# Optimization experiments

Hardware: AMD Instinct MI355X
Metric: run time of the kernel (lower is better)

## Reference

```python
import jax, jax.numpy as jnp
import numpy as np

B, S, H = 2, 512, 768
NH, HD = 12, 64  # num heads, head size


def setup_inputs() -> dict:
    key = jax.random.key(0)
    ks = jax.random.split(key, 11)
    std = 0.02
    return {
        "from_path_hidden": jax.random.normal(ks[0], (B, S, H), jnp.float32),
        "to_path_hidden": jax.random.normal(ks[1], (B, S, H), jnp.float32),
        "attention_mask": jnp.zeros((B, 1, 1, S), jnp.float32),
        "Wq": jax.random.normal(ks[2], (H, H), jnp.float32) * std,
        "bq": jnp.zeros((H,), jnp.float32),
        "Wk": jax.random.normal(ks[3], (H, H), jnp.float32) * std,
        "bk": jnp.zeros((H,), jnp.float32),
        "Wvf": jax.random.normal(ks[4], (H, H), jnp.float32) * std,
        "bvf": jnp.zeros((H,), jnp.float32),
        "Wvt": jax.random.normal(ks[5], (H, H), jnp.float32) * std,
        "bvt": jnp.zeros((H,), jnp.float32),
    }


def _heads(x):
    # [B,S,H] -> [B,NH,S,HD]
    b, s, _ = x.shape
    return x.reshape(b, s, NH, HD).transpose(0, 2, 1, 3)


def reference(from_path_hidden, to_path_hidden, attention_mask,
              Wq, bq, Wk, bk, Wvf, bvf, Wvt, bvt):
    # torch Linear: y = x @ W^T + b
    q = _heads(from_path_hidden @ Wq.T + bq)   # [B,NH,S,HD]
    k = _heads(to_path_hidden @ Wk.T + bk)     # [B,NH,S,HD]
    vf = _heads(from_path_hidden @ Wvf.T + bvf)  # value_from, indexed by query pos
    vt = _heads(to_path_hidden @ Wvt.T + bvt)    # value_to, indexed by key pos

    scores = jnp.einsum("bhqd,bhkd->bhqk", q, k) / jnp.sqrt(jnp.asarray(HD, q.dtype))
    scores = scores + attention_mask  # additive mask, broadcasts [B,1,1,S]
    probs = jax.nn.softmax(scores, axis=-1)  # dropout is identity in eval mode

    # use_expanded_value=True: ctx[b,h,q,:] = sum_k probs[b,h,q,k] * (vf[b,h,q,:] + vt[b,h,k,:])
    # = probs @ vt + (sum_k probs) * vf  -- exact, avoids the [B,NH,S,S,HD] tensor
    ctx = jnp.einsum("bhqk,bhkd->bhqd", probs, vt) + probs.sum(-1, keepdims=True) * vf

    # [B,NH,S,HD] -> [B,S,H]
    ctx = ctx.transpose(0, 2, 1, 3).reshape(from_path_hidden.shape[0], -1, NH * HD)
    return ctx
```

## Files before the change

kernel.cpp:

```cpp
#include <hip/hip_runtime.h>
#include <hip/hip_bf16.h>
#include <math.h>

#define Bq  2
#define Sq  512
#define Hq  768
#define NHq 12
#define HDq 64
#define SHsz (Bq * Sq * Hq)
#define WSZ  (Hq * Hq)

typedef __bf16 bf16x8 __attribute__((ext_vector_type(8)));
typedef unsigned short u16x8 __attribute__((ext_vector_type(8)));
typedef float f32x4 __attribute__((ext_vector_type(4)));

static __device__ __forceinline__ unsigned short f2bf(float f) {
    unsigned int u = __float_as_uint(f);
    u += 0x7fffu + ((u >> 16) & 1u);
    return (unsigned short)(u >> 16);
}
static __device__ __forceinline__ float bf2f(unsigned short v) {
    return __uint_as_float(((unsigned int)v) << 16);
}

static __device__ __forceinline__ f32x4 mfma_bf16(bf16x8 a, bf16x8 b, f32x4 c) {
    return __builtin_amdgcn_mfma_f32_16x16x32_bf16(a, b, c, 0, 0, 0);
}

static __device__ __forceinline__ void async16(const void* g, void* l) {
    __builtin_amdgcn_global_load_lds(
        (const __attribute__((address_space(1))) void*)(uintptr_t)g,
        (__attribute__((address_space(3))) void*)(unsigned int)(uintptr_t)l,
        16, 0, 0);
}

__global__ __launch_bounds__(256) void cvt_kernel(
    const float* __restrict__ from_h, const float* __restrict__ to_h,
    const float* __restrict__ Wq, const float* __restrict__ Wk,
    const float* __restrict__ Wvf, const float* __restrict__ Wvt,
    unsigned short* __restrict__ ws)
{
    const int z = blockIdx.y;
    const float* src; unsigned short* dst; int n;
    switch (z) {
        case 0:  src = from_h; dst = ws + 3 * SHsz;           n = SHsz; break;
        case 1:  src = to_h;   dst = ws + 4 * SHsz;           n = SHsz; break;
        case 2:  src = Wq;     dst = ws + 5 * SHsz;           n = WSZ;  break;
        case 3:  src = Wk;     dst = ws + 5 * SHsz + WSZ;     n = WSZ;  break;
        case 4:  src = Wvf;    dst = ws + 5 * SHsz + 2 * WSZ; n = WSZ;  break;
        default: src = Wvt;    dst = ws + 5 * SHsz + 3 * WSZ; n = WSZ;  break;
    }
    const int idx = (blockIdx.x * 256 + threadIdx.x) * 8;
    if (idx < n) {
        const float4 a = *(const float4*)(src + idx);
        const float4 b = *(const float4*)(src + idx + 4);
        u16x8 o = { f2bf(a.x), f2bf(a.y), f2bf(a.z), f2bf(a.w),
                    f2bf(b.x), f2bf(b.y), f2bf(b.z), f2bf(b.w) };
        *(u16x8*)(dst + idx) = o;
    }
}

__global__ __launch_bounds__(256) void proj_gemm(
    const unsigned short* __restrict__ fbf, const unsigned short* __restrict__ tbf,
    const unsigned short* __restrict__ wqb, const unsigned short* __restrict__ wkb,
    const unsigned short* __restrict__ wvfb, const unsigned short* __restrict__ wvtb,
    const float* __restrict__ bq, const float* __restrict__ bk,
    const float* __restrict__ bvf, const float* __restrict__ bvt,
    unsigned short* __restrict__ qbf, unsigned short* __restrict__ kbf,
    unsigned short* __restrict__ vtt, unsigned short* __restrict__ vfb)
{
    __shared__ unsigned short lds[16384];
    unsigned short* Als = lds;
    unsigned short* Wls = lds + 8192;

    const int z = blockIdx.z;
    const unsigned short *A, *W;
    const float* bias;
    if (z == 0)      { A = fbf; W = wqb;  bias = bq;  }
    else if (z == 1) { A = tbf; W = wkb;  bias = bk;  }
    else if (z == 2) { A = tbf; W = wvtb; bias = bvt; }
    else             { A = fbf; W = wvfb; bias = bvf; }

    const int t    = threadIdx.x;
    const int wv   = t >> 6;
    const int lane = t & 63;
    const int l16  = lane & 15;
    const int quad = lane >> 4;
    const int bn = blockIdx.x;
    const int bm = blockIdx.y;

    const int srow = lane >> 3;
    const int sgrp = (lane & 7) ^ (srow & 7);

    f32x4 acc[4] = {};

    for (int kt = 0; kt < Hq / 128; ++kt) {
        __syncthreads();
        #pragma unroll
        for (int kh = 0; kh < 2; ++kh) {
            const int kc = kt * 128 + kh * 64;
            #pragma unroll
            for (int c = 0; c < 2; ++c) {
                const int r0 = wv * 16 + c * 8;
                async16(A + (size_t)(bm * 64 + r0 + srow) * Hq + kc + sgrp * 8, &Als[kh * 4096 + r0 * 64]);
                async16(W + (size_t)(bn * 64 + r0 + srow) * Hq + kc + sgrp * 8, &Wls[kh * 4096 + r0 * 64]);
            }
        }
        __syncthreads();

        #pragma unroll
        for (int kh = 0; kh < 2; ++kh) {
            #pragma unroll
            for (int kk = 0; kk < 2; ++kk) {
                const int sg = kh * 4096 + ((kk * 4 + quad) ^ (l16 & 7)) * 8;
                const bf16x8 af = *(const bf16x8*)&Als[(wv * 16 + l16) * 64 + sg];
                #pragma unroll
                for (int j = 0; j < 4; ++j) {
                    const bf16x8 bfr = *(const bf16x8*)&Wls[(j * 16 + l16) * 64 + sg];
                    acc[j] = mfma_bf16(af, bfr, acc[j]);
                }
            }
        }
    }

    __syncthreads();

    unsigned short* rep = lds;
    if (z == 2) {
        #pragma unroll
        for (int j = 0; j < 4; ++j) {
            const float bv = bias[bn * 64 + j * 16 + l16];
            #pragma unroll
            for (int r = 0; r < 4; ++r)
                rep[(j * 16 + l16) * 72 + wv * 16 + quad * 4 + r] = f2bf(acc[j][r] + bv);
        }
    } else {
        #pragma unroll
        for (int j = 0; j < 4; ++j) {
            const float bv = bias[bn * 64 + j * 16 + l16];
            #pragma unroll
            for (int r = 0; r < 4; ++r)
                rep[(wv * 16 + quad * 4 + r) * 72 + j * 16 + l16] = f2bf(acc[j][r] + bv);
        }
    }
    __syncthreads();

    const int row = t >> 2;
    #pragma unroll
    for (int p = 0; p < 2; ++p) {
        const int col0 = ((t & 3) + p * 4) * 8;
        const u16x8 v = *(const u16x8*)&rep[row * 72 + col0];
        if (z == 2) {
            const int bb = bm >> 3, m0 = (bm & 7) * 64;
            *(u16x8*)&vtt[((size_t)((bb * NHq + bn) * HDq + row)) * Sq + m0 + col0] = v;
        } else {
            unsigned short* dstp = (z == 0) ? qbf : (z == 1) ? kbf : vfb;
            *(u16x8*)&dstp[(size_t)(bm * 64 + row) * Hq + bn * 64 + col0] = v;
        }
    }
}

__global__ __launch_bounds__(256) void attn_kernel(
    const unsigned short* __restrict__ qbf,
    const unsigned short* __restrict__ kbf,
    const unsigned short* __restrict__ vtt,
    const unsigned short* __restrict__ vfb,
    const float* __restrict__ amask,
    float* __restrict__ outp)
{
    __shared__ unsigned short Plds[4 * 16 * 40];
    __shared__ float Ols[3 * 16 * 68];
    __shared__ float Tls[3 * 16];

    const int t    = threadIdx.x;
    const int wv   = t >> 6;
    const int lane = t & 63;
    const int l16  = lane & 15;
    const int quad = lane >> 4;
    const int q0 = blockIdx.x * 16;
    const int h  = blockIdx.y;
    const int b  = blockIdx.z;

    const unsigned short* qrow = qbf + ((size_t)(b * Sq + q0 + l16)) * Hq + h * HDq + quad * 8;
    const bf16x8 aq0 = *(const bf16x8*)qrow;
    const bf16x8 aq1 = *(const bf16x8*)(qrow + 32);

    f32x4 O[4] = {};
    float ts[4] = {0.f, 0.f, 0.f, 0.f};
    const float scale = 0.125f;
    unsigned short* myP = &Plds[wv * 16 * 40];

    for (int kt = 0; kt < 4; ++kt) {
        const int k0 = wv * 128 + kt * 32;
        const unsigned short* kr = kbf + ((size_t)(b * Sq + k0 + l16)) * Hq + h * HDq + quad * 8;
        const bf16x8 kb00 = *(const bf16x8*)kr;
        const bf16x8 kb01 = *(const bf16x8*)(kr + 32);
        const bf16x8 kb10 = *(const bf16x8*)(kr + 16 * Hq);
        const bf16x8 kb11 = *(const bf16x8*)(kr + 16 * Hq + 32);

        f32x4 s0 = {}, s1 = {};
        s0 = mfma_bf16(aq0, kb00, s0);
        s0 = mfma_bf16(aq1, kb01, s0);
        s1 = mfma_bf16(aq0, kb10, s1);
        s1 = mfma_bf16(aq1, kb11, s1);

        const float mk0 = amask[b * Sq + k0 + l16];
        const float mk1 = amask[b * Sq + k0 + 16 + l16];

        float p0[4], p1[4];
        #pragma unroll
        for (int r = 0; r < 4; ++r) {
            p0[r] = __expf(s0[r] * scale + mk0);
            p1[r] = __expf(s1[r] * scale + mk1);
            ts[r] += p0[r] + p1[r];
        }

        #pragma unroll
        for (int r = 0; r < 4; ++r) {
            myP[(quad * 4 + r) * 40 + l16]      = f2bf(p0[r]);
            myP[(quad * 4 + r) * 40 + 16 + l16] = f2bf(p1[r]);
        }
        const bf16x8 pa = *(const bf16x8*)&myP[l16 * 40 + quad * 8];

        const unsigned short* vr = vtt + ((size_t)((b * NHq + h) * HDq + l16)) * Sq + k0 + quad * 8;
        #pragma unroll
        for (int j = 0; j < 4; ++j) {
            const bf16x8 vb = *(const bf16x8*)(vr + (size_t)j * 16 * Sq);
            O[j] = mfma_bf16(pa, vb, O[j]);
        }
    }

    #pragma unroll
    for (int off = 1; off < 16; off <<= 1)
        #pragma unroll
        for (int r = 0; r < 4; ++r) ts[r] += __shfl_xor(ts[r], off);

    if (wv > 0) {
        float* myO = &Ols[(wv - 1) * 16 * 68];
        #pragma unroll
        for (int j = 0; j < 4; ++j)
            #pragma unroll
            for (int r = 0; r < 4; ++r)
                myO[(quad * 4 + r) * 68 + j * 16 + l16] = O[j][r];
        if (l16 == 0)
            #pragma unroll
            for (int r = 0; r < 4; ++r) Tls[(wv - 1) * 16 + quad * 4 + r] = ts[r];
    }
    __syncthreads();
    if (wv > 0) return;

    #pragma unroll
    for (int r = 0; r < 4; ++r) {
        const int rr = quad * 4 + r;
        const float tot = ts[r] + Tls[rr] + Tls[16 + rr] + Tls[32 + rr];
        const float inv = 1.f / tot;
        const int row = q0 + rr;
        #pragma unroll
        for (int j = 0; j < 4; ++j) {
            const int col = h * HDq + j * 16 + l16;
            const size_t idx = ((size_t)(b * Sq + row)) * Hq + col;
            const float oj = O[j][r]
                + Ols[rr * 68 + j * 16 + l16]
                + Ols[16 * 68 + rr * 68 + j * 16 + l16]
                + Ols[2 * 16 * 68 + rr * 68 + j * 16 + l16];
            outp[idx] = oj * inv + bf2f(vfb[idx]);
        }
    }
}

extern "C" void kernel_launch(void* const* d_in, const int* in_sizes, int n_in,
                              void* d_out, int out_size, void* d_ws, size_t ws_size,
                              hipStream_t stream) {
    (void)in_sizes; (void)n_in; (void)out_size; (void)ws_size;
    const float* from_h = (const float*)d_in[0];
    const float* to_h   = (const float*)d_in[1];
    const float* amask  = (const float*)d_in[2];
    const float* Wq  = (const float*)d_in[3];
    const float* bqv = (const float*)d_in[4];
    const float* Wk  = (const float*)d_in[5];
    const float* bkv = (const float*)d_in[6];
    const float* Wvf = (const float*)d_in[7];
    const float* bvf = (const float*)d_in[8];
    const float* Wvt = (const float*)d_in[9];
    const float* bvt = (const float*)d_in[10];
    float* outp = (float*)d_out;

    unsigned short* ws = (unsigned short*)d_ws;
    unsigned short* qbf = ws;
    unsigned short* kbf = ws + SHsz;
    unsigned short* vtt = ws + 2 * SHsz;
    unsigned short* fbf = ws + 3 * SHsz;
    unsigned short* tbf = ws + 4 * SHsz;
    unsigned short* wqb  = ws + 5 * SHsz;
    unsigned short* wkb  = wqb + WSZ;
    unsigned short* wvfb = wqb + 2 * WSZ;
    unsigned short* wvtb = wqb + 3 * WSZ;
    unsigned short* vfb  = wqb + 4 * WSZ;

    cvt_kernel<<<dim3(384, 6), 256, 0, stream>>>(from_h, to_h, Wq, Wk, Wvf, Wvt, ws);

    dim3 gp(12, 16, 4);
    proj_gemm<<<gp, 256, 0, stream>>>(fbf, tbf, wqb, wkb, wvfb, wvtb,
                                      bqv, bkv, bvf, bvt, qbf, kbf, vtt, vfb);

    dim3 ga(Sq / 16, NHq, Bq);
    attn_kernel<<<ga, 256, 0, stream>>>(qbf, kbf, vtt, vfb, amask, outp);
}
```

Baseline: 107.2 us.

## Fuse convert, projection, and attention into one persistent kernel with grid barriers

Replaces the three separate launches (bf16 conversion, projection GEMM, attention) with a single persistent kernel of 512 blocks. The stages are separated by software grid barriers built on atomic counters and spin-wait, and each stage distributes its work over the blocks in a strided loop. The aim is to remove launch overhead and inter-kernel gaps. In exchange it relies on all 512 blocks being co-resident and adds spin-barrier cost. The barrier has a timeout that could break correctness under contention, and the counter is never reset, relying on rounding to multiples of NBLK.

```diff
diff --git a/kernel.cpp b/kernel.cpp
--- a/kernel.cpp
+++ b/kernel.cpp
@@ -9,6 +9,7 @@
 #define HDq 64
 #define SHsz (Bq * Sq * Hq)
 #define WSZ  (Hq * Hq)
+#define NBLK 512
 
 typedef __bf16 bf16x8 __attribute__((ext_vector_type(8)));
 typedef unsigned short u16x8 __attribute__((ext_vector_type(8)));
@@ -34,236 +35,294 @@
         16, 0, 0);
 }
 
-__global__ __launch_bounds__(256) void cvt_kernel(
+static __device__ __forceinline__ u16x8 cvt8(float4 a, float4 b) {
+    u16x8 o = { f2bf(a.x), f2bf(a.y), f2bf(a.z), f2bf(a.w),
+                f2bf(b.x), f2bf(b.y), f2bf(b.z), f2bf(b.w) };
+    return o;
+}
+
+__device__ unsigned int g_bar[2] = {0u, 0u};
+
+static __device__ __forceinline__ void grid_barrier(int which) {
+    __threadfence();
+    __syncthreads();
+    if (threadIdx.x == 0) {
+        const unsigned int v =
+            __hip_atomic_fetch_add(&g_bar[which], 1u, __ATOMIC_ACQ_REL,
+                                   __HIP_MEMORY_SCOPE_AGENT) + 1u;
+        const unsigned int target = ((v + (NBLK - 1u)) / NBLK) * NBLK;
+        const long long t0 = (long long)__builtin_amdgcn_s_memrealtime();
+        while (__hip_atomic_load(&g_bar[which], __ATOMIC_ACQUIRE,
+                                 __HIP_MEMORY_SCOPE_AGENT) < target) {
+            __builtin_amdgcn_s_sleep(2);
+            if ((long long)__builtin_amdgcn_s_memrealtime() - t0 > 4000000LL) break;
+        }
+    }
+    __syncthreads();
+    __threadfence();
+}
+
+__global__ __launch_bounds__(256, 2) void fused_kernel(
     const float* __restrict__ from_h, const float* __restrict__ to_h,
-    const float* __restrict__ Wq, const float* __restrict__ Wk,
-    const float* __restrict__ Wvf, const float* __restrict__ Wvt,
-    unsigned short* __restrict__ ws)
-{
-    const int z = blockIdx.y;
-    const float* src; unsigned short* dst; int n;
-    switch (z) {
-        case 0:  src = from_h; dst = ws + 3 * SHsz;           n = SHsz; break;
-        case 1:  src = to_h;   dst = ws + 4 * SHsz;           n = SHsz; break;
-        case 2:  src = Wq;     dst = ws + 5 * SHsz;           n = WSZ;  break;
-        case 3:  src = Wk;     dst = ws + 5 * SHsz + WSZ;     n = WSZ;  break;
-        case 4:  src = Wvf;    dst = ws + 5 * SHsz + 2 * WSZ; n = WSZ;  break;
-        default: src = Wvt;    dst = ws + 5 * SHsz + 3 * WSZ; n = WSZ;  break;
-    }
-    const int idx = (blockIdx.x * 256 + threadIdx.x) * 8;
-    if (idx < n) {
-        const float4 a = *(const float4*)(src + idx);
-        const float4 b = *(const float4*)(src + idx + 4);
-        u16x8 o = { f2bf(a.x), f2bf(a.y), f2bf(a.z), f2bf(a.w),
-                    f2bf(b.x), f2bf(b.y), f2bf(b.z), f2bf(b.w) };
-        *(u16x8*)(dst + idx) = o;
-    }
-}
-
-__global__ __launch_bounds__(256) void proj_gemm(
-    const unsigned short* __restrict__ fbf, const unsigned short* __restrict__ tbf,
-    const unsigned short* __restrict__ wqb, const unsigned short* __restrict__ wkb,
-    const unsigned short* __restrict__ wvfb, const unsigned short* __restrict__ wvtb,
-    const float* __restrict__ bq, const float* __restrict__ bk,
-    const float* __restrict__ bvf, const float* __restrict__ bvt,
-    unsigned short* __restrict__ qbf, unsigned short* __restrict__ kbf,
-    unsigned short* __restrict__ vtt, unsigned short* __restrict__ vfb)
+    const float* __restrict__ amask,
+    const float* __restrict__ Wq,  const float* __restrict__ bq,
+    const float* __restrict__ Wk,  const float* __restrict__ bk,
+    const float* __restrict__ Wvf, const float* __restrict__ bvf,
+    const float* __restrict__ Wvt, const float* __restrict__ bvt,
+    float* __restrict__ outp, unsigned short* __restrict__ ws)
 {
     __shared__ unsigned short lds[16384];
-    unsigned short* Als = lds;
-    unsigned short* Wls = lds + 8192;
-
-    const int z = blockIdx.z;
-    const unsigned short *A, *W;
-    const float* bias;
-    if (z == 0)      { A = fbf; W = wqb;  bias = bq;  }
-    else if (z == 1) { A = tbf; W = wkb;  bias = bk;  }
-    else if (z == 2) { A = tbf; W = wvtb; bias = bvt; }
-    else             { A = fbf; W = wvfb; bias = bvf; }
-
-    const int t    = threadIdx.x;
-    const int wv   = t >> 6;
-    const int lane = t & 63;
-    const int l16  = lane & 15;
-    const int quad = lane >> 4;
-    const int bn = blockIdx.x;
-    const int bm = blockIdx.y;
-
-    const int srow = lane >> 3;
-    const int sgrp = (lane & 7) ^ (srow & 7);
-
-    f32x4 acc[4] = {};
-
-    for (int kt = 0; kt < Hq / 128; ++kt) {
+
+    unsigned short* qbf  = ws;
+    unsigned short* kbf  = ws + SHsz;
+    unsigned short* vtt  = ws + 2 * SHsz;
+    unsigned short* fbf  = ws + 3 * SHsz;
+    unsigned short* tbf  = ws + 4 * SHsz;
+    unsigned short* wqb  = ws + 5 * SHsz;
+    unsigned short* vfb  = wqb + 4 * WSZ;
+
+    const int bid = blockIdx.x;
+    const int t   = threadIdx.x;
+
+    if (bid < 128) {
+        const int g0 = bid * 256 + t;
+        #pragma unroll
+        for (int it = 0; it < 3; ++it) {
+            const int idx = (g0 + it * 32768) * 8;
+            const float4 a = *(const float4*)(from_h + idx);
+            const float4 b = *(const float4*)(from_h + idx + 4);
+            *(u16x8*)(fbf + idx) = cvt8(a, b);
+        }
+    } else if (bid < 256) {
+        const int g0 = (bid - 128) * 256 + t;
+        #pragma unroll
+        for (int it = 0; it < 3; ++it) {
+            const int idx = (g0 + it * 32768) * 8;
+            const float4 a = *(const float4*)(to_h + idx);
+            const float4 b = *(const float4*)(to_h + idx + 4);
+            *(u16x8*)(tbf + idx) = cvt8(a, b);
+        }
+    } else {
+        const int g0 = (bid - 256) * 256 + t;
+        #pragma unroll
+        for (int it = 0; it < 4; ++it) {
+            const int c  = g0 + it * 65536;
+            const int wi = c / 73728;
+            const int off = c - wi * 73728;
+            const float* src = (wi == 0) ? Wq : (wi == 1) ? Wk : (wi == 2) ? Wvf : Wvt;
+            const float4 a = *(const float4*)(src + off * 8);
+            const float4 b = *(const float4*)(src + off * 8 + 4);
+            *(u16x8*)(wqb + c * 8) = cvt8(a, b);
+        }
+        if (g0 < 32768) {
+            const int c  = g0 + 262144;
+            const int off = c - 3 * 73728;
+            const float4 a = *(const float4*)(Wvt + off * 8);
+            const float4 b = *(const float4*)(Wvt + off * 8 + 4);
+            *(u16x8*)(wqb + c * 8) = cvt8(a, b);
+        }
+    }
+
+    grid_barrier(0);
+
+    for (int wid = bid; wid < 768; wid += NBLK) {
+        unsigned short* Als = lds;
+        unsigned short* Wls = lds + 8192;
+
+        const int z  = wid / 192;
+        const int r  = wid - z * 192;
+        const int bm = r / 12;
+        const int bn = r - bm * 12;
+
+        const unsigned short *A, *W;
+        const float* bias;
+        if (z == 0)      { A = fbf; W = wqb;           bias = bq;  }
+        else if (z == 1) { A = tbf; W = wqb + WSZ;     bias = bk;  }
+        else if (z == 2) { A = tbf; W = wqb + 3 * WSZ; bias = bvt; }
+        else             { A = fbf; W = wqb + 2 * WSZ; bias = bvf; }
+
+        const int wv   = t >> 6;
+        const int lane = t & 63;
+        const int l16  = lane & 15;
+        const int quad = lane >> 4;
+        const int srow = lane >> 3;
+        const int sgrp = (lane & 7) ^ (srow & 7);
+
+        f32x4 acc[4] = {};
+
+        for (int kt = 0; kt < Hq / 128; ++kt) {
+            __syncthreads();
+            #pragma unroll
+            for (int kh = 0; kh < 2; ++kh) {
+                const int kc = kt * 128 + kh * 64;
+                #pragma unroll
+                for (int c = 0; c < 2; ++c) {
+                    const int r0 = wv * 16 + c * 8;
+                    async16(A + (size_t)(bm * 64 + r0 + srow) * Hq + kc + sgrp * 8, &Als[kh * 4096 + r0 * 64]);
+                    async16(W + (size_t)(bn * 64 + r0 + srow) * Hq + kc + sgrp * 8, &Wls[kh * 4096 + r0 * 64]);
+                }
+            }
+            __syncthreads();
+
+            #pragma unroll
+            for (int kh = 0; kh < 2; ++kh) {
+                #pragma unroll
+                for (int kk = 0; kk < 2; ++kk) {
+                    const int sg = kh * 4096 + ((kk * 4 + quad) ^ (l16 & 7)) * 8;
+                    const bf16x8 af = *(const bf16x8*)&Als[(wv * 16 + l16) * 64 + sg];
+                    #pragma unroll
+                    for (int j = 0; j < 4; ++j) {
+                        const bf16x8 bfr = *(const bf16x8*)&Wls[(j * 16 + l16) * 64 + sg];
+                        acc[j] = mfma_bf16(af, bfr, acc[j]);
+                    }
+                }
+            }
+        }
+
         __syncthreads();
+
+        unsigned short* rep = lds;
+        if (z == 2) {
+            #pragma unroll
+            for (int j = 0; j < 4; ++j) {
+                const float bv = bias[bn * 64 + j * 16 + l16];
+                #pragma unroll
+                for (int r2 = 0; r2 < 4; ++r2)
+                    rep[(j * 16 + l16) * 72 + wv * 16 + quad * 4 + r2] = f2bf(acc[j][r2] + bv);
+            }
+        } else {
+            #pragma unroll
+            for (int j = 0; j < 4; ++j) {
+                const float bv = bias[bn * 64 + j * 16 + l16];
+                #pragma unroll
+                for (int r2 = 0; r2 < 4; ++r2)
+                    rep[(wv * 16 + quad * 4 + r2) * 72 + j * 16 + l16] = f2bf(acc[j][r2] + bv);
+            }
+        }
+        __syncthreads();
+
+        const int row = t >> 2;
         #pragma unroll
-        for (int kh = 0; kh < 2; ++kh) {
-            const int kc = kt * 128 + kh * 64;
-            #pragma unroll
-            for (int c = 0; c < 2; ++c) {
-                const int r0 = wv * 16 + c * 8;
-                async16(A + (size_t)(bm * 64 + r0 + srow) * Hq + kc + sgrp * 8, &Als[kh * 4096 + r0 * 64]);
-                async16(W + (size_t)(bn * 64 + r0 + srow) * Hq + kc + sgrp * 8, &Wls[kh * 4096 + r0 * 64]);
+        for (int p = 0; p < 2; ++p) {
+            const int col0 = ((t & 3) + p * 4) * 8;
+            const u16x8 v = *(const u16x8*)&rep[row * 72 + col0];
+            if (z == 2) {
+                const int bb = bm >> 3, m0 = (bm & 7) * 64;
+                *(u16x8*)&vtt[((size_t)((bb * NHq + bn) * HDq + row)) * Sq + m0 + col0] = v;
+            } else {
+                unsigned short* dstp = (z == 0) ? qbf : (z == 1) ? kbf : vfb;
+                *(u16x8*)&dstp[(size_t)(bm * 64 + row) * Hq + bn * 64 + col0] = v;
             }
         }
         __syncthreads();
-
-        #pragma unroll
-        for (int kh = 0; kh < 2; ++kh) {
-            #pragma unroll
-            for (int kk = 0; kk < 2; ++kk) {
-                const int sg = kh * 4096 + ((kk * 4 + quad) ^ (l16 & 7)) * 8;
-                const bf16x8 af = *(const bf16x8*)&Als[(wv * 16 + l16) * 64 + sg];
+    }
+
+    grid_barrier(1);
+
+    {
+        unsigned short* Plds = lds;
+        float* Ols = (float*)(lds + 2560);
+        float* Tls = (float*)(lds + 2560 + 6528);
+
+        const int wv   = t >> 6;
+        const int lane = t & 63;
+        const int l16  = lane & 15;
+        const int quad = lane >> 4;
+        const float scale = 0.125f;
+        unsigned short* myP = &Plds[wv * 16 * 40];
+
+        for (int wid = bid; wid < 768; wid += NBLK) {
+            __syncthreads();
+
+            const int b  = wid / 384;
+            const int r3 = wid - b * 384;
+            const int h  = r3 >> 5;
+            const int q0 = (r3 & 31) * 16;
+
+            const unsigned short* qrow = qbf + ((size_t)(b * Sq + q0 + l16)) * Hq + h * HDq + quad * 8;
+            const bf16x8 aq0 = *(const bf16x8*)qrow;
+            const bf16x8 aq1 = *(const bf16x8*)(qrow + 32);
+
+            f32x4 O[4] = {};
+            float ts[4] = {0.f, 0.f, 0.f, 0.f};
+
+            for (int kt = 0; kt < 4; ++kt) {
+                const int k0 = wv * 128 + kt * 32;
+                const unsigned short* kr = kbf + ((size_t)(b * Sq + k0 + l16)) * Hq + h * HDq + quad * 8;
+                const bf16x8 kb00 = *(const bf16x8*)kr;
+                const bf16x8 kb01 = *(const bf16x8*)(kr + 32);
+                const bf16x8 kb10 = *(const bf16x8*)(kr + 16 * Hq);
+                const bf16x8 kb11 = *(const bf16x8*)(kr + 16 * Hq + 32);
+
+                f32x4 s0 = {}, s1 = {};
+                s0 = mfma_bf16(aq0, kb00, s0);
+                s0 = mfma_bf16(aq1, kb01, s0);
+                s1 = mfma_bf16(aq0, kb10, s1);
+                s1 = mfma_bf16(aq1, kb11, s1);
+
+                const float mk0 = amask[b * Sq + k0 + l16];
+                const float mk1 = amask[b * Sq + k0 + 16 + l16];
+
+                float p0[4], p1[4];
+                #pragma unroll
+                for (int r2 = 0; r2 < 4; ++r2) {
+                    p0[r2] = __expf(s0[r2] * scale + mk0);
+                    p1[r2] = __expf(s1[r2] * scale + mk1);
+                    ts[r2] += p0[r2] + p1[r2];
+                }
+
+                #pragma unroll
+                for (int r2 = 0; r2 < 4; ++r2) {
+                    myP[(quad * 4 + r2) * 40 + l16]      = f2bf(p0[r2]);
+                    myP[(quad * 4 + r2) * 40 + 16 + l16] = f2bf(p1[r2]);
+                }
+                const bf16x8 pa = *(const bf16x8*)&myP[l16 * 40 + quad * 8];
+
+                const unsigned short* vr = vtt + ((size_t)((b * NHq + h) * HDq + l16)) * Sq + k0 + quad * 8;
                 #pragma unroll
                 for (int j = 0; j < 4; ++j) {
-                    const bf16x8 bfr = *(const bf16x8*)&Wls[(j * 16 + l16) * 64 + sg];
-                    acc[j] = mfma_bf16(af, bfr, acc[j]);
-                }
-            }
-        }
-    }
-
-    __syncthreads();
-
-    unsigned short* rep = lds;
-    if (z == 2) {
-        #pragma unroll
-        for (int j = 0; j < 4; ++j) {
-            const float bv = bias[bn * 64 + j * 16 + l16];
-            #pragma unroll
-            for (int r = 0; r < 4; ++r)
-                rep[(j * 16 + l16) * 72 + wv * 16 + quad * 4 + r] = f2bf(acc[j][r] + bv);
-        }
-    } else {
-        #pragma unroll
-        for (int j = 0; j < 4; ++j) {
-            const float bv = bias[bn * 64 + j * 16 + l16];
-            #pragma unroll
-            for (int r = 0; r < 4; ++r)
-                rep[(wv * 16 + quad * 4 + r) * 72 + j * 16 + l16] = f2bf(acc[j][r] + bv);
-        }
-    }
-    __syncthreads();
-
-    const int row = t >> 2;
-    #pragma unroll
-    for (int p = 0; p < 2; ++p) {
-        const int col0 = ((t & 3) + p * 4) * 8;
-        const u16x8 v = *(const u16x8*)&rep[row * 72 + col0];
-        if (z == 2) {
-            const int bb = bm >> 3, m0 = (bm & 7) * 64;
-            *(u16x8*)&vtt[((size_t)((bb * NHq + bn) * HDq + row)) * Sq + m0 + col0] = v;
-        } else {
-            unsigned short* dstp = (z == 0) ? qbf : (z == 1) ? kbf : vfb;
-            *(u16x8*)&dstp[(size_t)(bm * 64 + row) * Hq + bn * 64 + col0] = v;
-        }
-    }
-}
-
-__global__ __launch_bounds__(256) void attn_kernel(
-    const unsigned short* __restrict__ qbf,
-    const unsigned short* __restrict__ kbf,
-    const unsigned short* __restrict__ vtt,
-    const unsigned short* __restrict__ vfb,
-    const float* __restrict__ amask,
-    float* __restrict__ outp)
-{
-    __shared__ unsigned short Plds[4 * 16 * 40];
-    __shared__ float Ols[3 * 16 * 68];
-    __shared__ float Tls[3 * 16];
-
-    const int t    = threadIdx.x;
-    const int wv   = t >> 6;
-    const int lane = t & 63;
-    const int l16  = lane & 15;
-    const int quad = lane >> 4;
-    const int q0 = blockIdx.x * 16;
-    const int h  = blockIdx.y;
-    const int b  = blockIdx.z;
-
-    const unsigned short* qrow = qbf + ((size_t)(b * Sq + q0 + l16)) * Hq + h * HDq + quad * 8;
-    const bf16x8 aq0 = *(const bf16x8*)qrow;
-    const bf16x8 aq1 = *(const bf16x8*)(qrow + 32);
-
-    f32x4 O[4] = {};
-    float ts[4] = {0.f, 0.f, 0.f, 0.f};
-    const float scale = 0.125f;
-    unsigned short* myP = &Plds[wv * 16 * 40];
-
-    for (int kt = 0; kt < 4; ++kt) {
-        const int k0 = wv * 128 + kt * 32;
-        const unsigned short* kr = kbf + ((size_t)(b * Sq + k0 + l16)) * Hq + h * HDq + quad * 8;
-        const bf16x8 kb00 = *(const bf16x8*)kr;
-        const bf16x8 kb01 = *(const bf16x8*)(kr + 32);
-        const bf16x8 kb10 = *(const bf16x8*)(kr + 16 * Hq);
-        const bf16x8 kb11 = *(const bf16x8*)(kr + 16 * Hq + 32);
-
-        f32x4 s0 = {}, s1 = {};
-        s0 = mfma_bf16(aq0, kb00, s0);
-        s0 = mfma_bf16(aq1, kb01, s0);
-        s1 = mfma_bf16(aq0, kb10, s1);
-        s1 = mfma_bf16(aq1, kb11, s1);
-
-        const float mk0 = amask[b * Sq + k0 + l16];
-        const float mk1 = amask[b * Sq + k0 + 16 + l16];
-
-        float p0[4], p1[4];
-        #pragma unroll
-        for (int r = 0; r < 4; ++r) {
-            p0[r] = __expf(s0[r] * scale + mk0);
-            p1[r] = __expf(s1[r] * scale + mk1);
-            ts[r] += p0[r] + p1[r];
-        }
-
-        #pragma unroll
-        for (int r = 0; r < 4; ++r) {
-            myP[(quad * 4 + r) * 40 + l16]      = f2bf(p0[r]);
-            myP[(quad * 4 + r) * 40 + 16 + l16] = f2bf(p1[r]);
-        }
-        const bf16x8 pa = *(const bf16x8*)&myP[l16 * 40 + quad * 8];
-
-        const unsigned short* vr = vtt + ((size_t)((b * NHq + h) * HDq + l16)) * Sq + k0 + quad * 8;
-        #pragma unroll
-        for (int j = 0; j < 4; ++j) {
-            const bf16x8 vb = *(const bf16x8*)(vr + (size_t)j * 16 * Sq);
-            O[j] = mfma_bf16(pa, vb, O[j]);
-        }
-    }
-
-    #pragma unroll
-    for (int off = 1; off < 16; off <<= 1)
-        #pragma unroll
-        for (int r = 0; r < 4; ++r) ts[r] += __shfl_xor(ts[r], off);
-
-    if (wv > 0) {
-        float* myO = &Ols[(wv - 1) * 16 * 68];
-        #pragma unroll
-        for (int j = 0; j < 4; ++j)
-            #pragma unroll
-            for (int r = 0; r < 4; ++r)
-                myO[(quad * 4 + r) * 68 + j * 16 + l16] = O[j][r];
-        if (l16 == 0)
-            #pragma unroll
-            for (int r = 0; r < 4; ++r) Tls[(wv - 1) * 16 + quad * 4 + r] = ts[r];
-    }
-    __syncthreads();
-    if (wv > 0) return;
-
-    #pragma unroll
-    for (int r = 0; r < 4; ++r) {
-        const int rr = quad * 4 + r;
-        const float tot = ts[r] + Tls[rr] + Tls[16 + rr] + Tls[32 + rr];
-        const float inv = 1.f / tot;
-        const int row = q0 + rr;
-        #pragma unroll
-        for (int j = 0; j < 4; ++j) {
-            const int col = h * HDq + j * 16 + l16;
-            const size_t idx = ((size_t)(b * Sq + row)) * Hq + col;
-            const float oj = O[j][r]
-                + Ols[rr * 68 + j * 16 + l16]
-                + Ols[16 * 68 + rr * 68 + j * 16 + l16]
-                + Ols[2 * 16 * 68 + rr * 68 + j * 16 + l16];
-            outp[idx] = oj * inv + bf2f(vfb[idx]);
+                    const bf16x8 vb = *(const bf16x8*)(vr + (size_t)j * 16 * Sq);
+                    O[j] = mfma_bf16(pa, vb, O[j]);
+                }
+            }
+
+            #pragma unroll
+            for (int off = 1; off < 16; off <<= 1)
+                #pragma unroll
+                for (int r2 = 0; r2 < 4; ++r2) ts[r2] += __shfl_xor(ts[r2], off);
+
+            if (wv > 0) {
+                float* myO = &Ols[(wv - 1) * 16 * 68];
+                #pragma unroll
+                for (int j = 0; j < 4; ++j)
+                    #pragma unroll
+                    for (int r2 = 0; r2 < 4; ++r2)
+                        myO[(quad * 4 + r2) * 68 + j * 16 + l16] = O[j][r2];
+                if (l16 == 0)
+                    #pragma unroll
+                    for (int r2 = 0; r2 < 4; ++r2) Tls[(wv - 1) * 16 + quad * 4 + r2] = ts[r2];
+            }
+            __syncthreads();
+
+            if (wv == 0) {
+                #pragma unroll
+                for (int r2 = 0; r2 < 4; ++r2) {
+                    const int rr = quad * 4 + r2;
+                    const float tot = ts[r2] + Tls[rr] + Tls[16 + rr] + Tls[32 + rr];
+                    const float inv = 1.f / tot;
+                    const int row = q0 + rr;
+                    #pragma unroll
+                    for (int j = 0; j < 4; ++j) {
+                        const int col = h * HDq + j * 16 + l16;
+                        const size_t idx = ((size_t)(b * Sq + row)) * Hq + col;
+                        const float oj = O[j][r2]
+                            + Ols[rr * 68 + j * 16 + l16]
+                            + Ols[16 * 68 + rr * 68 + j * 16 + l16]
+                            + Ols[2 * 16 * 68 + rr * 68 + j * 16 + l16];
+                        outp[idx] = oj * inv + bf2f(vfb[idx]);
+                    }
+                }
+            }
         }
     }
 }
@@ -284,25 +343,8 @@
     const float* Wvt = (const float*)d_in[9];
     const float* bvt = (const float*)d_in[10];
     float* outp = (float*)d_out;
-
     unsigned short* ws = (unsigned short*)d_ws;
-    unsigned short* qbf = ws;
-    unsigned short* kbf = ws + SHsz;
-    unsigned short* vtt = ws + 2 * SHsz;
-    unsigned short* fbf = ws + 3 * SHsz;
-    unsigned short* tbf = ws + 4 * SHsz;
-    unsigned short* wqb  = ws + 5 * SHsz;
-    unsigned short* wkb  = wqb + WSZ;
-    unsigned short* wvfb = wqb + 2 * WSZ;
-    unsigned short* wvtb = wqb + 3 * WSZ;
-    unsigned short* vfb  = wqb + 4 * WSZ;
-
-    cvt_kernel<<<dim3(384, 6), 256, 0, stream>>>(from_h, to_h, Wq, Wk, Wvf, Wvt, ws);
-
-    dim3 gp(12, 16, 4);
-    proj_gemm<<<gp, 256, 0, stream>>>(fbf, tbf, wqb, wkb, wvfb, wvtb,
-                                      bqv, bkv, bvf, bvt, qbf, kbf, vtt, vfb);
-
-    dim3 ga(Sq / 16, NHq, Bq);
-    attn_kernel<<<ga, 256, 0, stream>>>(qbf, kbf, vtt, vfb, amask, outp);
-}
+
+    fused_kernel<<<dim3(NBLK), dim3(256), 0, stream>>>(
+        from_h, to_h, amask, Wq, bqv, Wk, bkv, Wvf, bvf, Wvt, bvt, outp, ws);
+}
```

Measured after the change: 390.0 us. 264% more time.
